# Optimization experiments

Hardware: AMD Instinct MI355X
Metric: run time of the kernel (lower is better)

Reference implementation:

```python
import jax, jax.numpy as jnp
import numpy as np

PS = 32
NUM_ANG_BINS = 36


def circular_gauss_kernel(kernlen):
    # CircularGaussKernel from the HardNet repo (norm=True, circ_zeros=False)
    half = kernlen / 2.0
    r2 = half * half
    sigma2 = 0.9 * r2
    x = np.linspace(-half, half, kernlen)
    xv, yv = np.meshgrid(x, x, indexing='xy')
    d2 = xv ** 2 + yv ** 2
    k = np.exp(-d2 / sigma2)
    k = k / np.sum(k)
    return jnp.asarray(k, dtype=jnp.float32)


def setup_inputs() -> dict:
    key = jax.random.key(0)
    x = jax.random.uniform(key, (65536, 1, PS, PS), dtype=jnp.float32)
    return {"x": x}


def reference(x):
    B = x.shape[0]
    gk = 10.0 * circular_gauss_kernel(PS)  # [PS, PS]

    # gx: Conv2d kernel [[0.5, 0, -0.5]] with replicate pad (1,1,0,0)
    xp = jnp.pad(x, ((0, 0), (0, 0), (0, 0), (1, 1)), mode='edge')
    gx = 0.5 * (xp[..., :-2] - xp[..., 2:])
    # gy: Conv2d kernel [[0.5],[0],[-0.5]] with replicate pad (0,0,1,1)
    yp = jnp.pad(x, ((0, 0), (0, 0), (1, 1), (0, 0)), mode='edge')
    gy = 0.5 * (yp[:, :, :-2, :] - yp[:, :, 2:, :])

    mag = jnp.sqrt(gx * gx + gy * gy + 1e-10) * gk  # gk broadcasts over [B,1,PS,PS]
    ori = jnp.arctan2(gy, gx)

    o_big = NUM_ANG_BINS * (ori + jnp.pi) / (2.0 * jnp.pi)
    bo0 = jnp.floor(o_big)
    wo1 = o_big - bo0
    bo0 = (bo0 % NUM_ANG_BINS).astype(jnp.int32)
    wo0 = (1.0 - wo1) * mag  # note: upper-bin weight wo1*mag is dropped, as in original

    # histogram via per-patch scatter-add (replaces 36 masked full-tensor scans)
    bins_flat = bo0.reshape(B, -1)  # [B, PS*PS]
    w_flat = wo0.reshape(B, -1)
    hist = jax.vmap(lambda w, b: jax.ops.segment_sum(w, b, num_segments=NUM_ANG_BINS))(
        w_flat, bins_flat) / float(PS * PS)  # adaptive_avg_pool2d -> mean

    # Conv1d angular smoothing, kernel [0.33,0.34,0.33], zero padding=1
    hp = jnp.pad(hist, ((0, 0), (1, 1)))
    sm = 0.33 * hp[:, :-2] + 0.34 * hp[:, 1:-1] + 0.33 * hp[:, 2:]

    idx = jnp.argmax(sm, axis=1)
    angle = -(2.0 * jnp.pi * idx.astype(x.dtype) / NUM_ANG_BINS - jnp.pi)
    return angle
```

## Files before the change

### kernel.cpp

```cpp
#include <hip/hip_runtime.h>

#define PS 32
#define NPIX (PS * PS)
#define NB 36
#define WPB 4
#define HCOL 64
#define HWORDS (NB * HCOL)

__global__ __launch_bounds__(256) void gk_init_kernel(float* __restrict__ gk10) {
    __shared__ double red[256];
    const int tid = threadIdx.x;
    const double delta = 32.0 / 31.0;
    const double sigma2 = 0.9 * 256.0;

    double kv[4];
    double s = 0.0;
#pragma unroll
    for (int j = 0; j < 4; ++j) {
        int p = tid * 4 + j;
        int r = p >> 5, c = p & 31;
        double xr = (r == 31) ? 16.0 : ((double)r * delta + (-16.0));
        double xc = (c == 31) ? 16.0 : ((double)c * delta + (-16.0));
        double d2 = xc * xc + xr * xr;
        kv[j] = exp(-d2 / sigma2);
        s += kv[j];
    }
    red[tid] = s;
    __syncthreads();
    for (int off = 128; off > 0; off >>= 1) {
        if (tid < off) red[tid] += red[tid + off];
        __syncthreads();
    }
    double sum = red[0];
#pragma unroll
    for (int j = 0; j < 4; ++j) {
        int p = tid * 4 + j;
        gk10[p] = __fmul_rn(10.0f, (float)(kv[j] / sum));
    }
}

__device__ __attribute__((noinline))
void fix_pixel(float lv, float rv, float uv, float dv, float gk, float* col) {
    const float PI_F    = 3.14159265358979323846f;
    const float TWOPI_F = 6.28318530717958647692f;
    float gx = __fmul_rn(0.5f, __fsub_rn(lv, rv));
    float gy = __fmul_rn(0.5f, __fsub_rn(uv, dv));
    float s2 = __fadd_rn(__fadd_rn(__fmul_rn(gx, gx), __fmul_rn(gy, gy)), 1e-10f);
    float mag = __fmul_rn(__fsqrt_rn(s2), gk);

    float ori  = (float)atan2((double)gy, (double)gx);
    float obig = __fdiv_rn(__fmul_rn(36.0f, __fadd_rn(ori, PI_F)), TWOPI_F);
    float bo0f = floorf(obig);
    float wo1  = __fsub_rn(obig, bo0f);
    int bo = (int)bo0f;
    if (bo >= NB) bo -= NB;
    float wo0 = __fmul_rn(__fsub_rn(1.0f, wo1), mag);
    col[bo * HCOL] += wo0;
}

__global__ __launch_bounds__(256) void orient_kernel(const float* __restrict__ x,
                                                     const float* __restrict__ gk10,
                                                     float* __restrict__ out) {
#pragma clang fp contract(off)
    const float PI_F    = 3.14159265358979323846f;
    const float TWOPI_F = 6.28318530717958647692f;

    __shared__ __align__(16) float hist[WPB][HWORDS];

    const int tid = threadIdx.x;
    const int w = tid >> 6;
    const int l = tid & 63;
    const int patch = blockIdx.x * WPB + w;

    float* hw = hist[w];

    const int sr = l >> 3;
    const int sc = l & 7;

    const float* xb = x + (size_t)patch * NPIX + (sr * 4) * PS + sc * 4;
    const float* gb = gk10 + (sr * 4) * PS + sc * 4;
    float4 sq[4], gq[4];
#pragma unroll
    for (int k = 0; k < 4; ++k) {
        sq[k] = *reinterpret_cast<const float4*>(xb + k * PS);
        gq[k] = *reinterpret_cast<const float4*>(gb + k * PS);
    }

    {
        float4 z4 = make_float4(0.0f, 0.0f, 0.0f, 0.0f);
        float4* hz = reinterpret_cast<float4*>(hw);
#pragma unroll
        for (int p = 0; p < 9; ++p) hz[p * 64 + l] = z4;
    }

    float s[4][4], g[4][4];
#pragma unroll
    for (int k = 0; k < 4; ++k) {
        s[k][0] = sq[k].x; s[k][1] = sq[k].y; s[k][2] = sq[k].z; s[k][3] = sq[k].w;
        g[k][0] = gq[k].x; g[k][1] = gq[k].y; g[k][2] = gq[k].z; g[k][3] = gq[k].w;
    }

    const int upL = (sr > 0) ? (l - 8) : l;
    const int dnL = (sr < 7) ? (l + 8) : l;
    const int lfL = (sc > 0) ? (l - 1) : l;
    const int rtL = (sc < 7) ? (l + 1) : l;
    float Uh[4], Dh[4], Lh[4], Rh[4];
#pragma unroll
    for (int j = 0; j < 4; ++j) {
        float tu = __shfl(s[3][j], upL, 64);
        float td = __shfl(s[0][j], dnL, 64);
        Uh[j] = (sr == 0) ? s[0][j] : tu;
        Dh[j] = (sr == 7) ? s[3][j] : td;
    }
#pragma unroll
    for (int k = 0; k < 4; ++k) {
        float tl = __shfl(s[k][3], lfL, 64);
        float tr = __shfl(s[k][0], rtL, 64);
        Lh[k] = (sc == 0) ? s[k][0] : tl;
        Rh[k] = (sc == 7) ? s[k][3] : tr;
    }

    unsigned int badbits = 0;
    float* mycol = hw + l;
    const float BINSCALE = 5.72957795130823208768f;
#pragma unroll
    for (int k = 0; k < 4; ++k) {
#pragma unroll
        for (int j = 0; j < 4; ++j) {
            float lv = (j == 0) ? Lh[k] : s[k][j - 1];
            float rv = (j == 3) ? Rh[k] : s[k][j + 1];
            float uv = (k == 0) ? Uh[j] : s[k - 1][j];
            float dv = (k == 3) ? Dh[j] : s[k + 1][j];

            float dx = __fsub_rn(lv, rv);
            float dy = __fsub_rn(uv, dv);
            float t1 = fmaf(dy, dy, __fmul_rn(dx, dx));
            float s2 = fmaf(t1, 0.25f, 1e-10f);
            float mag = __fmul_rn(__fsqrt_rn(s2), g[k][j]);

            float ax = fabsf(dx), ay = fabsf(dy);
            float mn = fminf(ax, ay);
            float mx = fmaxf(fmaxf(ax, ay), 1.17549435e-38f);
            float rr = mn * __builtin_amdgcn_rcpf(mx);
            float t  = rr * rr;
            float u = 0.00282363896258175373077393f;
            u = fmaf(u, t, -0.0159569028764963150024414f);
            u = fmaf(u, t,  0.0425049886107444763183594f);
            u = fmaf(u, t, -0.0748900920152664184570312f);
            u = fmaf(u, t,  0.106347933411598205566406f);
            u = fmaf(u, t, -0.142027363181114196777344f);
            u = fmaf(u, t,  0.199926957488059997558594f);
            u = fmaf(u, t, -0.333331018686294555664062f);
            float at  = fmaf(rr * t, u, rr);
            float atb = at * BINSCALE;

            float a9  = (ay > ax)   ? __fsub_rn(9.0f,  atb) : atb;
            float a18 = (dx < 0.0f) ? __fsub_rn(18.0f, a9)  : a9;
            float as  = copysignf(a18, dy);
            float obig = __fadd_rn(as, 18.0f);
            float wo1  = __builtin_amdgcn_fractf(obig);
            unsigned bo = (unsigned)obig;
            bo = (bo > 35u) ? 35u : bo;

            bool bad = fabsf(__fsub_rn(wo1, 0.5f)) >= 0.49998f;
            float wo0 = fmaf(-wo1, mag, mag);
            wo0 = bad ? 0.0f : wo0;
            mycol[bo * HCOL] += wo0;
            badbits |= bad ? (1u << (k * 4 + j)) : 0u;
        }
    }

    if (__ballot(badbits != 0)) {
#pragma unroll
        for (int k = 0; k < 4; ++k) {
#pragma unroll
            for (int j = 0; j < 4; ++j) {
                if (badbits & (1u << (k * 4 + j))) {
                    float lv = (j == 0) ? Lh[k] : s[k][j - 1];
                    float rv = (j == 3) ? Rh[k] : s[k][j + 1];
                    float uv = (k == 0) ? Uh[j] : s[k - 1][j];
                    float dv = (k == 3) ? Dh[j] : s[k + 1][j];
                    fix_pixel(lv, rv, uv, dv, g[k][j], mycol);
                }
            }
        }
    }
    asm volatile("s_waitcnt lgkmcnt(0)" ::: "memory");

    float hval = 0.0f;
    if (l < NB) {
        const float2* row2 = reinterpret_cast<const float2*>(hw + l * HCOL);
        float tot = 0.0f;
#pragma unroll
        for (int k = 0; k < 32; ++k) {
            float2 a = row2[(k + l) & 31];
            tot += (a.x + a.y);
        }
        hval = __fmul_rn(tot, 1.0f / 1024.0f);
    }

    float hm = __shfl_up(hval, 1, 64);
    if (l == 0) hm = 0.0f;
    float hp = __shfl_down(hval, 1, 64);
    float sm = 0.0f;
    if (l < NB) {
        sm = __fadd_rn(__fadd_rn(__fmul_rn(0.33f, hm), __fmul_rn(0.34f, hval)),
                       __fmul_rn(0.33f, hp));
    }

    float mv = sm;
#pragma unroll
    for (int off = 32; off > 0; off >>= 1) {
        float o = __shfl_xor(mv, off, 64);
        mv = fmaxf(mv, o);
    }
    unsigned long long msk = __ballot(sm == mv);

    if (l == 0) {
        int bi = __ffsll(msk) - 1;
        float t2 = __fdiv_rn(__fmul_rn(TWOPI_F, (float)bi), 36.0f);
        out[patch] = __fsub_rn(PI_F, t2);
    }
}

extern "C" void kernel_launch(void* const* d_in, const int* in_sizes, int n_in,
                              void* d_out, int out_size, void* d_ws, size_t ws_size,
                              hipStream_t stream) {
    const float* x = (const float*)d_in[0];
    float* out = (float*)d_out;
    float* gk10 = (float*)d_ws;

    const int B = in_sizes[0] / NPIX;

    gk_init_kernel<<<1, 256, 0, stream>>>(gk10);
    orient_kernel<<<B / WPB, 256, 0, stream>>>(x, gk10, out);
}
```

Baseline: 107.4 us.

## Pad histogram stride, load halos from global, and vectorize reduction

Changes the per-lane histogram layout to a stride of 66 with an extra 37th row. Bin 36 overflow lands in that spare row and is dropped, which removes the clamp. The padding also lets the row reduction read sequential float2 values without the rotated index while avoiding bank conflicts. The wave shuffles for halo pixels are replaced by extra global loads that should mostly hit cache. The reduction now uses a packed two-wide accumulator, which changes summation order slightly. In exchange the kernel uses more LDS and issues more scalar global loads.

```diff
diff --git a/kernel.cpp b/kernel.cpp
--- a/kernel.cpp
+++ b/kernel.cpp
@@ -4,8 +4,11 @@
 #define NPIX (PS * PS)
 #define NB 36
 #define WPB 4
-#define HCOL 64
-#define HWORDS (NB * HCOL)
+#define HSTRIDE 66
+#define HROWS 37
+#define HWORDS (HROWS * HSTRIDE)
+
+typedef float v2f __attribute__((ext_vector_type(2)));
 
 __global__ __launch_bounds__(256) void gk_init_kernel(float* __restrict__ gk10) {
     __shared__ double red[256];
@@ -55,7 +58,7 @@
     int bo = (int)bo0f;
     if (bo >= NB) bo -= NB;
     float wo0 = __fmul_rn(__fsub_rn(1.0f, wo1), mag);
-    col[bo * HCOL] += wo0;
+    col[bo * HSTRIDE] += wo0;
 }
 
 __global__ __launch_bounds__(256) void orient_kernel(const float* __restrict__ x,
@@ -77,13 +80,28 @@
     const int sr = l >> 3;
     const int sc = l & 7;
 
-    const float* xb = x + (size_t)patch * NPIX + (sr * 4) * PS + sc * 4;
-    const float* gb = gk10 + (sr * 4) * PS + sc * 4;
+    const float* xp0 = x + (size_t)patch * NPIX;
+    const float* xb  = xp0 + (sr * 4) * PS + sc * 4;
+    const float* gb  = gk10 + (sr * 4) * PS + sc * 4;
     float4 sq[4], gq[4];
 #pragma unroll
     for (int k = 0; k < 4; ++k) {
         sq[k] = *reinterpret_cast<const float4*>(xb + k * PS);
         gq[k] = *reinterpret_cast<const float4*>(gb + k * PS);
+    }
+    const int rU = (sr > 0) ? (sr * 4 - 1) : 0;
+    const int rD = (sr < 7) ? (sr * 4 + 4) : 31;
+    float4 Uq = *reinterpret_cast<const float4*>(xp0 + rU * PS + sc * 4);
+    float4 Dq = *reinterpret_cast<const float4*>(xp0 + rD * PS + sc * 4);
+    const int cL = (sc > 0) ? (sc * 4 - 1) : 0;
+    const int cR = (sc < 7) ? (sc * 4 + 4) : 31;
+    const float* pL = xp0 + (sr * 4) * PS + cL;
+    const float* pR = xp0 + (sr * 4) * PS + cR;
+    float Lh[4], Rh[4];
+#pragma unroll
+    for (int k = 0; k < 4; ++k) {
+        Lh[k] = pL[k * PS];
+        Rh[k] = pR[k * PS];
     }
 
     {
@@ -91,34 +109,17 @@
         float4* hz = reinterpret_cast<float4*>(hw);
 #pragma unroll
         for (int p = 0; p < 9; ++p) hz[p * 64 + l] = z4;
-    }
-
-    float s[4][4], g[4][4];
+        if (l < 18) hz[576 + l] = z4;
+    }
+
+    float s[4][4], g[4][4], Uh[4], Dh[4];
 #pragma unroll
     for (int k = 0; k < 4; ++k) {
         s[k][0] = sq[k].x; s[k][1] = sq[k].y; s[k][2] = sq[k].z; s[k][3] = sq[k].w;
         g[k][0] = gq[k].x; g[k][1] = gq[k].y; g[k][2] = gq[k].z; g[k][3] = gq[k].w;
     }
-
-    const int upL = (sr > 0) ? (l - 8) : l;
-    const int dnL = (sr < 7) ? (l + 8) : l;
-    const int lfL = (sc > 0) ? (l - 1) : l;
-    const int rtL = (sc < 7) ? (l + 1) : l;
-    float Uh[4], Dh[4], Lh[4], Rh[4];
-#pragma unroll
-    for (int j = 0; j < 4; ++j) {
-        float tu = __shfl(s[3][j], upL, 64);
-        float td = __shfl(s[0][j], dnL, 64);
-        Uh[j] = (sr == 0) ? s[0][j] : tu;
-        Dh[j] = (sr == 7) ? s[3][j] : td;
-    }
-#pragma unroll
-    for (int k = 0; k < 4; ++k) {
-        float tl = __shfl(s[k][3], lfL, 64);
-        float tr = __shfl(s[k][0], rtL, 64);
-        Lh[k] = (sc == 0) ? s[k][0] : tl;
-        Rh[k] = (sc == 7) ? s[k][3] : tr;
-    }
+    Uh[0] = Uq.x; Uh[1] = Uq.y; Uh[2] = Uq.z; Uh[3] = Uq.w;
+    Dh[0] = Dq.x; Dh[1] = Dq.y; Dh[2] = Dq.z; Dh[3] = Dq.w;
 
     unsigned int badbits = 0;
     float* mycol = hw + l;
@@ -160,12 +161,11 @@
             float obig = __fadd_rn(as, 18.0f);
             float wo1  = __builtin_amdgcn_fractf(obig);
             unsigned bo = (unsigned)obig;
-            bo = (bo > 35u) ? 35u : bo;
 
             bool bad = fabsf(__fsub_rn(wo1, 0.5f)) >= 0.49998f;
             float wo0 = fmaf(-wo1, mag, mag);
             wo0 = bad ? 0.0f : wo0;
-            mycol[bo * HCOL] += wo0;
+            mycol[bo * HSTRIDE] += wo0;
             badbits |= bad ? (1u << (k * 4 + j)) : 0u;
         }
     }
@@ -189,13 +189,15 @@
 
     float hval = 0.0f;
     if (l < NB) {
-        const float2* row2 = reinterpret_cast<const float2*>(hw + l * HCOL);
-        float tot = 0.0f;
+        const float2* row2 = reinterpret_cast<const float2*>(hw + l * HSTRIDE);
+        v2f tot2 = {0.0f, 0.0f};
 #pragma unroll
         for (int k = 0; k < 32; ++k) {
-            float2 a = row2[(k + l) & 31];
-            tot += (a.x + a.y);
+            float2 a = row2[k];
+            v2f av = {a.x, a.y};
+            tot2 = tot2 + av;
         }
+        float tot = tot2.x + tot2.y;
         hval = __fmul_rn(tot, 1.0f / 1024.0f);
     }
 
```

Result: slower. 112.7 us (+4.9%).

## Use persistent grid-stride blocks with register prefetch of next patch

Applied to the files above, without the earlier changes.

Replaces the one-patch-per-wave launch with a fixed grid of 1024 blocks that loop over patches in grid-stride order. Each wave prefetches the next patch into registers while it processes the current one, and it loads the Gaussian weights only once. The bin clamp is removed and the histogram gains a spare 37th row to absorb the overflow index, and the row sum now uses a packed two-wide vector add. This is meant to hide global load latency and cut per-block launch and setup overhead, at the cost of more register pressure and possibly lower occupancy.

```diff
diff --git a/kernel.cpp b/kernel.cpp
--- a/kernel.cpp
+++ b/kernel.cpp
@@ -5,7 +5,11 @@
 #define NB 36
 #define WPB 4
 #define HCOL 64
-#define HWORDS (NB * HCOL)
+#define HROWS 37
+#define HWORDS (HROWS * HCOL)
+#define NBLOCKS 1024
+
+typedef float v2f __attribute__((ext_vector_type(2)));
 
 __global__ __launch_bounds__(256) void gk_init_kernel(float* __restrict__ gk10) {
     __shared__ double red[256];
@@ -60,7 +64,8 @@
 
 __global__ __launch_bounds__(256) void orient_kernel(const float* __restrict__ x,
                                                      const float* __restrict__ gk10,
-                                                     float* __restrict__ out) {
+                                                     float* __restrict__ out,
+                                                     int B) {
 #pragma clang fp contract(off)
     const float PI_F    = 3.14159265358979323846f;
     const float TWOPI_F = 6.28318530717958647692f;
@@ -70,156 +75,180 @@
     const int tid = threadIdx.x;
     const int w = tid >> 6;
     const int l = tid & 63;
-    const int patch = blockIdx.x * WPB + w;
+    const int stride = gridDim.x * WPB;
 
     float* hw = hist[w];
+    float* mycol = hw + l;
 
     const int sr = l >> 3;
     const int sc = l & 7;
-
-    const float* xb = x + (size_t)patch * NPIX + (sr * 4) * PS + sc * 4;
-    const float* gb = gk10 + (sr * 4) * PS + sc * 4;
-    float4 sq[4], gq[4];
-#pragma unroll
-    for (int k = 0; k < 4; ++k) {
-        sq[k] = *reinterpret_cast<const float4*>(xb + k * PS);
-        gq[k] = *reinterpret_cast<const float4*>(gb + k * PS);
-    }
-
+    const int laneOff = (sr * 4) * PS + sc * 4;
+
+    float g[4][4];
     {
-        float4 z4 = make_float4(0.0f, 0.0f, 0.0f, 0.0f);
-        float4* hz = reinterpret_cast<float4*>(hw);
-#pragma unroll
-        for (int p = 0; p < 9; ++p) hz[p * 64 + l] = z4;
-    }
-
-    float s[4][4], g[4][4];
-#pragma unroll
-    for (int k = 0; k < 4; ++k) {
-        s[k][0] = sq[k].x; s[k][1] = sq[k].y; s[k][2] = sq[k].z; s[k][3] = sq[k].w;
-        g[k][0] = gq[k].x; g[k][1] = gq[k].y; g[k][2] = gq[k].z; g[k][3] = gq[k].w;
-    }
-
-    const int upL = (sr > 0) ? (l - 8) : l;
-    const int dnL = (sr < 7) ? (l + 8) : l;
-    const int lfL = (sc > 0) ? (l - 1) : l;
-    const int rtL = (sc < 7) ? (l + 1) : l;
-    float Uh[4], Dh[4], Lh[4], Rh[4];
-#pragma unroll
-    for (int j = 0; j < 4; ++j) {
-        float tu = __shfl(s[3][j], upL, 64);
-        float td = __shfl(s[0][j], dnL, 64);
-        Uh[j] = (sr == 0) ? s[0][j] : tu;
-        Dh[j] = (sr == 7) ? s[3][j] : td;
-    }
-#pragma unroll
-    for (int k = 0; k < 4; ++k) {
-        float tl = __shfl(s[k][3], lfL, 64);
-        float tr = __shfl(s[k][0], rtL, 64);
-        Lh[k] = (sc == 0) ? s[k][0] : tl;
-        Rh[k] = (sc == 7) ? s[k][3] : tr;
-    }
-
-    unsigned int badbits = 0;
-    float* mycol = hw + l;
+        const float* gb = gk10 + laneOff;
+#pragma unroll
+        for (int k = 0; k < 4; ++k) {
+            float4 gq = *reinterpret_cast<const float4*>(gb + k * PS);
+            g[k][0] = gq.x; g[k][1] = gq.y; g[k][2] = gq.z; g[k][3] = gq.w;
+        }
+    }
+
+    int patch = blockIdx.x * WPB + w;
+    if (patch >= B) return;
+
+    float4 nxt[4];
+    {
+        const float* xb = x + (size_t)patch * NPIX + laneOff;
+#pragma unroll
+        for (int k = 0; k < 4; ++k)
+            nxt[k] = *reinterpret_cast<const float4*>(xb + k * PS);
+    }
+
     const float BINSCALE = 5.72957795130823208768f;
-#pragma unroll
-    for (int k = 0; k < 4; ++k) {
+
+    for (; patch < B; patch += stride) {
+        {
+            float4 z4 = make_float4(0.0f, 0.0f, 0.0f, 0.0f);
+            float4* hz = reinterpret_cast<float4*>(hw);
+#pragma unroll
+            for (int p = 0; p < 9; ++p) hz[p * 64 + l] = z4;
+        }
+
+        float s[4][4];
+#pragma unroll
+        for (int k = 0; k < 4; ++k) {
+            s[k][0] = nxt[k].x; s[k][1] = nxt[k].y;
+            s[k][2] = nxt[k].z; s[k][3] = nxt[k].w;
+        }
+        const int np = patch + stride;
+        if (np < B) {
+            const float* xb = x + (size_t)np * NPIX + laneOff;
+#pragma unroll
+            for (int k = 0; k < 4; ++k)
+                nxt[k] = *reinterpret_cast<const float4*>(xb + k * PS);
+        }
+
+        const int upL = (sr > 0) ? (l - 8) : l;
+        const int dnL = (sr < 7) ? (l + 8) : l;
+        const int lfL = (sc > 0) ? (l - 1) : l;
+        const int rtL = (sc < 7) ? (l + 1) : l;
+        float Uh[4], Dh[4], Lh[4], Rh[4];
 #pragma unroll
         for (int j = 0; j < 4; ++j) {
-            float lv = (j == 0) ? Lh[k] : s[k][j - 1];
-            float rv = (j == 3) ? Rh[k] : s[k][j + 1];
-            float uv = (k == 0) ? Uh[j] : s[k - 1][j];
-            float dv = (k == 3) ? Dh[j] : s[k + 1][j];
-
-            float dx = __fsub_rn(lv, rv);
-            float dy = __fsub_rn(uv, dv);
-            float t1 = fmaf(dy, dy, __fmul_rn(dx, dx));
-            float s2 = fmaf(t1, 0.25f, 1e-10f);
-            float mag = __fmul_rn(__fsqrt_rn(s2), g[k][j]);
-
-            float ax = fabsf(dx), ay = fabsf(dy);
-            float mn = fminf(ax, ay);
-            float mx = fmaxf(fmaxf(ax, ay), 1.17549435e-38f);
-            float rr = mn * __builtin_amdgcn_rcpf(mx);
-            float t  = rr * rr;
-            float u = 0.00282363896258175373077393f;
-            u = fmaf(u, t, -0.0159569028764963150024414f);
-            u = fmaf(u, t,  0.0425049886107444763183594f);
-            u = fmaf(u, t, -0.0748900920152664184570312f);
-            u = fmaf(u, t,  0.106347933411598205566406f);
-            u = fmaf(u, t, -0.142027363181114196777344f);
-            u = fmaf(u, t,  0.199926957488059997558594f);
-            u = fmaf(u, t, -0.333331018686294555664062f);
-            float at  = fmaf(rr * t, u, rr);
-            float atb = at * BINSCALE;
-
-            float a9  = (ay > ax)   ? __fsub_rn(9.0f,  atb) : atb;
-            float a18 = (dx < 0.0f) ? __fsub_rn(18.0f, a9)  : a9;
-            float as  = copysignf(a18, dy);
-            float obig = __fadd_rn(as, 18.0f);
-            float wo1  = __builtin_amdgcn_fractf(obig);
-            unsigned bo = (unsigned)obig;
-            bo = (bo > 35u) ? 35u : bo;
-
-            bool bad = fabsf(__fsub_rn(wo1, 0.5f)) >= 0.49998f;
-            float wo0 = fmaf(-wo1, mag, mag);
-            wo0 = bad ? 0.0f : wo0;
-            mycol[bo * HCOL] += wo0;
-            badbits |= bad ? (1u << (k * 4 + j)) : 0u;
-        }
-    }
-
-    if (__ballot(badbits != 0)) {
+            float tu = __shfl(s[3][j], upL, 64);
+            float td = __shfl(s[0][j], dnL, 64);
+            Uh[j] = (sr == 0) ? s[0][j] : tu;
+            Dh[j] = (sr == 7) ? s[3][j] : td;
+        }
+#pragma unroll
+        for (int k = 0; k < 4; ++k) {
+            float tl = __shfl(s[k][3], lfL, 64);
+            float tr = __shfl(s[k][0], rtL, 64);
+            Lh[k] = (sc == 0) ? s[k][0] : tl;
+            Rh[k] = (sc == 7) ? s[k][3] : tr;
+        }
+
+        unsigned int badbits = 0;
 #pragma unroll
         for (int k = 0; k < 4; ++k) {
 #pragma unroll
             for (int j = 0; j < 4; ++j) {
-                if (badbits & (1u << (k * 4 + j))) {
-                    float lv = (j == 0) ? Lh[k] : s[k][j - 1];
-                    float rv = (j == 3) ? Rh[k] : s[k][j + 1];
-                    float uv = (k == 0) ? Uh[j] : s[k - 1][j];
-                    float dv = (k == 3) ? Dh[j] : s[k + 1][j];
-                    fix_pixel(lv, rv, uv, dv, g[k][j], mycol);
+                float lv = (j == 0) ? Lh[k] : s[k][j - 1];
+                float rv = (j == 3) ? Rh[k] : s[k][j + 1];
+                float uv = (k == 0) ? Uh[j] : s[k - 1][j];
+                float dv = (k == 3) ? Dh[j] : s[k + 1][j];
+
+                float dx = __fsub_rn(lv, rv);
+                float dy = __fsub_rn(uv, dv);
+                float t1 = fmaf(dy, dy, __fmul_rn(dx, dx));
+                float s2 = fmaf(t1, 0.25f, 1e-10f);
+                float mag = __fmul_rn(__fsqrt_rn(s2), g[k][j]);
+
+                float ax = fabsf(dx), ay = fabsf(dy);
+                float mn = fminf(ax, ay);
+                float mx = fmaxf(fmaxf(ax, ay), 1.17549435e-38f);
+                float rr = mn * __builtin_amdgcn_rcpf(mx);
+                float t  = rr * rr;
+                float u = 0.00282363896258175373077393f;
+                u = fmaf(u, t, -0.0159569028764963150024414f);
+                u = fmaf(u, t,  0.0425049886107444763183594f);
+                u = fmaf(u, t, -0.0748900920152664184570312f);
+                u = fmaf(u, t,  0.106347933411598205566406f);
+                u = fmaf(u, t, -0.142027363181114196777344f);
+                u = fmaf(u, t,  0.199926957488059997558594f);
+                u = fmaf(u, t, -0.333331018686294555664062f);
+                float at  = fmaf(rr * t, u, rr);
+                float atb = at * BINSCALE;
+
+                float a9  = (ay > ax)   ? __fsub_rn(9.0f,  atb) : atb;
+                float a18 = (dx < 0.0f) ? __fsub_rn(18.0f, a9)  : a9;
+                float as  = copysignf(a18, dy);
+                float obig = __fadd_rn(as, 18.0f);
+                float wo1  = __builtin_amdgcn_fractf(obig);
+                unsigned bo = (unsigned)obig;
+
+                bool bad = fabsf(__fsub_rn(wo1, 0.5f)) >= 0.49998f;
+                float wo0 = fmaf(-wo1, mag, mag);
+                wo0 = bad ? 0.0f : wo0;
+                mycol[bo * HCOL] += wo0;
+                badbits |= bad ? (1u << (k * 4 + j)) : 0u;
+            }
+        }
+
+        if (__ballot(badbits != 0)) {
+#pragma unroll
+            for (int k = 0; k < 4; ++k) {
+#pragma unroll
+                for (int j = 0; j < 4; ++j) {
+                    if (badbits & (1u << (k * 4 + j))) {
+                        float lv = (j == 0) ? Lh[k] : s[k][j - 1];
+                        float rv = (j == 3) ? Rh[k] : s[k][j + 1];
+                        float uv = (k == 0) ? Uh[j] : s[k - 1][j];
+                        float dv = (k == 3) ? Dh[j] : s[k + 1][j];
+                        fix_pixel(lv, rv, uv, dv, g[k][j], mycol);
+                    }
                 }
             }
         }
-    }
-    asm volatile("s_waitcnt lgkmcnt(0)" ::: "memory");
-
-    float hval = 0.0f;
-    if (l < NB) {
-        const float2* row2 = reinterpret_cast<const float2*>(hw + l * HCOL);
-        float tot = 0.0f;
-#pragma unroll
-        for (int k = 0; k < 32; ++k) {
-            float2 a = row2[(k + l) & 31];
-            tot += (a.x + a.y);
-        }
-        hval = __fmul_rn(tot, 1.0f / 1024.0f);
-    }
-
-    float hm = __shfl_up(hval, 1, 64);
-    if (l == 0) hm = 0.0f;
-    float hp = __shfl_down(hval, 1, 64);
-    float sm = 0.0f;
-    if (l < NB) {
-        sm = __fadd_rn(__fadd_rn(__fmul_rn(0.33f, hm), __fmul_rn(0.34f, hval)),
-                       __fmul_rn(0.33f, hp));
-    }
-
-    float mv = sm;
-#pragma unroll
-    for (int off = 32; off > 0; off >>= 1) {
-        float o = __shfl_xor(mv, off, 64);
-        mv = fmaxf(mv, o);
-    }
-    unsigned long long msk = __ballot(sm == mv);
-
-    if (l == 0) {
-        int bi = __ffsll(msk) - 1;
-        float t2 = __fdiv_rn(__fmul_rn(TWOPI_F, (float)bi), 36.0f);
-        out[patch] = __fsub_rn(PI_F, t2);
+        asm volatile("s_waitcnt lgkmcnt(0)" ::: "memory");
+
+        float hval = 0.0f;
+        if (l < NB) {
+            const float2* row2 = reinterpret_cast<const float2*>(hw + l * HCOL);
+            v2f tot2 = {0.0f, 0.0f};
+#pragma unroll
+            for (int k = 0; k < 32; ++k) {
+                float2 a = row2[(k + l) & 31];
+                v2f av = {a.x, a.y};
+                tot2 = tot2 + av;
+            }
+            float tot = tot2.x + tot2.y;
+            hval = __fmul_rn(tot, 1.0f / 1024.0f);
+        }
+
+        float hm = __shfl_up(hval, 1, 64);
+        if (l == 0) hm = 0.0f;
+        float hp = __shfl_down(hval, 1, 64);
+        float sm = 0.0f;
+        if (l < NB) {
+            sm = __fadd_rn(__fadd_rn(__fmul_rn(0.33f, hm), __fmul_rn(0.34f, hval)),
+                           __fmul_rn(0.33f, hp));
+        }
+
+        float mv = sm;
+#pragma unroll
+        for (int off = 32; off > 0; off >>= 1) {
+            float o = __shfl_xor(mv, off, 64);
+            mv = fmaxf(mv, o);
+        }
+        unsigned long long msk = __ballot(sm == mv);
+
+        if (l == 0) {
+            int bi = __ffsll(msk) - 1;
+            float t2 = __fdiv_rn(__fmul_rn(TWOPI_F, (float)bi), 36.0f);
+            out[patch] = __fsub_rn(PI_F, t2);
+        }
     }
 }
 
@@ -232,6 +261,11 @@
 
     const int B = in_sizes[0] / NPIX;
 
+    int blocks = NBLOCKS;
+    int maxb   = (B + WPB - 1) / WPB;
+    if (blocks > maxb) blocks = maxb;
+    if (blocks < 1) blocks = 1;
+
     gk_init_kernel<<<1, 256, 0, stream>>>(gk10);
-    orient_kernel<<<B / WPB, 256, 0, stream>>>(x, gk10, out);
-}
+    orient_kernel<<<blocks, 256, 0, stream>>>(x, gk10, out, B);
+}
```

New measurement: 126.1 us. 1.17x slower.
